# Performance work log

Measured on AMD Instinct MI355X. Metric: run time of the kernel, lower is better.

Reference implementation:

```python
import jax, jax.numpy as jnp
import numpy as np

NUM_HEADS = 16
HEAD_DIM = 64  # v_emb_out // num_heads


def setup_inputs() -> dict:
    key = jax.random.key(0)
    ks = jax.random.split(key, 12)
    B, QL, KL = 2, 2048, 2048
    D = 1024  # q_emb_in = k_emb_in = v_emb_in = v_emb_out
    s = 0.02
    return {
        "q": jax.random.normal(ks[0], (B, QL, D), jnp.float32),
        "k": jax.random.normal(ks[1], (B, KL, D), jnp.float32),
        "v": jax.random.normal(ks[2], (B, KL, D), jnp.float32),
        "mask": jnp.zeros((B, 1, 1, KL), jnp.int32),
        "Wq": jax.random.normal(ks[3], (D, D), jnp.float32) * s,
        "bq": jnp.zeros((D,), jnp.float32),
        "Wk": jax.random.normal(ks[4], (D, D), jnp.float32) * s,
        "bk": jnp.zeros((D,), jnp.float32),
        "Wv": jax.random.normal(ks[5], (D, D), jnp.float32) * s,
        "bv": jnp.zeros((D,), jnp.float32),
        "Wo": jax.random.normal(ks[6], (D, D), jnp.float32) * s,
        "bo": jnp.zeros((D,), jnp.float32),
    }


def _split_heads(x):
    # (B, S, D) -> (B, H, S, Hd)
    B, S, D = x.shape
    return x.reshape(B, S, NUM_HEADS, HEAD_DIM).transpose(0, 2, 1, 3)


def reference(q, k, v, mask, Wq, bq, Wk, bk, Wv, bv, Wo, bo):
    Q = _split_heads(q @ Wq.T + bq)
    K = _split_heads(k @ Wk.T + bk)
    V = _split_heads(v @ Wv.T + bv)
    scores = jnp.einsum("bhqd,bhkd->bhqk", Q, K) / jnp.sqrt(
        jnp.asarray(HEAD_DIM, Q.dtype)
    )
    scores = jnp.where(mask.astype(bool), jnp.asarray(-jnp.inf, scores.dtype), scores)
    attn = jax.nn.softmax(scores, axis=-1)
    out = jnp.einsum("bhqk,bhkd->bhqd", attn, V)  # (B,H,Q,Hd)
    B, H, QL, Hd = out.shape
    out = out.transpose(0, 2, 1, 3).reshape(B, QL, H * Hd)
    return out @ Wo.T + bo
```

## Files before the change

### kernel.cpp

```cpp
#include <hip/hip_runtime.h>
#include <hip/hip_bf16.h>
#include <math.h>
#include <stdint.h>


typedef __bf16 bf16x8 __attribute__((ext_vector_type(8)));
typedef float  f32x4  __attribute__((ext_vector_type(4)));
typedef float  f32x8  __attribute__((ext_vector_type(8)));
typedef float  f32x16 __attribute__((ext_vector_type(16)));
typedef unsigned int   u32x4 __attribute__((ext_vector_type(4)));
typedef unsigned short u16x8 __attribute__((ext_vector_type(8)));
typedef unsigned short u16x4 __attribute__((ext_vector_type(4)));
typedef u16x8 u16x8a __attribute__((may_alias));
typedef u16x4 u16x4a __attribute__((may_alias));
typedef f32x8 f32x8a __attribute__((may_alias));
typedef unsigned short u16a __attribute__((may_alias));
typedef float f32a __attribute__((may_alias));

#define BATCH 2
#define SQL   2048
#define DM    1024
#define NH    16
#define HD    64

__device__ __forceinline__ unsigned short f2bf(float f) {
    union { __hip_bfloat16 h; unsigned short u; } cv;
    cv.h = __float2bfloat16(f);
    return cv.u;
}
__device__ __forceinline__ float bf2f(unsigned short u) {
    union { unsigned int i; float f; } cv;
    cv.i = ((unsigned int)u) << 16;
    return cv.f;
}
__device__ __forceinline__ bf16x8 ldfrag(const unsigned short* p) {
    return __builtin_bit_cast(bf16x8, *(const u16x8a*)p);
}
__device__ __forceinline__ void stage8(const void* __restrict__ src, size_t off,
                                       int f32f, unsigned short* dst) {
    if (f32f) {
        f32x8 v = *(const f32x8a*)((const float*)src + off);
        u16x8 o;
#pragma unroll
        for (int i = 0; i < 8; i++) o[i] = f2bf(v[i]);
        *(u16x8a*)dst = o;
    } else {
        *(u16x8a*)dst = *(const u16x8a*)((const unsigned short*)src + off);
    }
}
__device__ __forceinline__ float rdel(const void* p, size_t i, int f) {
    return f ? ((const f32a*)p)[i] : bf2f(((const u16a*)p)[i]);
}
__device__ __forceinline__ void gload16(const void* g, void* l) {
    __builtin_amdgcn_global_load_lds(
        (const __attribute__((address_space(1))) unsigned int*)g,
        (__attribute__((address_space(3))) unsigned int*)l,
        16, 0, 0);
}
__device__ __forceinline__ unsigned int cvtpk(float lo, float hi) {
    unsigned int r;
    asm("v_cvt_pk_bf16_f32 %0, %1, %2" : "=v"(r) : "v"(lo), "v"(hi));
    return r;
}
__device__ __forceinline__ float fexp2(float x) {
#if __has_builtin(__builtin_amdgcn_exp2f)
    return __builtin_amdgcn_exp2f(x);
#else
    float r;
    asm("v_exp_f32 %0, %1" : "=v"(r) : "v"(x));
    return r;
#endif
}

__global__ void sniff(const void* __restrict__ q, int* __restrict__ flag) {
    __shared__ int cnt;
    if (threadIdx.x == 0) cnt = 0;
    __syncthreads();
    const u16a* p = (const u16a*)q;
    int c = 0;
#pragma unroll
    for (int i = 0; i < 8; i++) {
        unsigned short u = p[threadIdx.x * 8 + i];
        int e = (u >> 7) & 0xFF;
        if (e >= 96 && e <= 159) c++;
    }
    atomicAdd(&cnt, c);
    __syncthreads();
    if (threadIdx.x == 0) *flag = (cnt < 1741) ? 1 : 0;
}

__global__ __launch_bounds__(256)
void convert(const void* s0, const void* s1, const void* s2, const void* s3,
             const void* s4, const void* s5, const void* s6,
             unsigned short* d0, unsigned short* d1, unsigned short* d2,
             unsigned short* d3, unsigned short* d4, unsigned short* d5,
             unsigned short* d6, const int* __restrict__ flag)
{
    if (*flag == 0) return;
    const int z = blockIdx.z;
    const float* s; unsigned short* d; size_t n;
    switch (z) {
        case 0: s = (const float*)s0; d = d0; n = (size_t)BATCH * SQL * DM; break;
        case 1: s = (const float*)s1; d = d1; n = (size_t)BATCH * SQL * DM; break;
        case 2: s = (const float*)s2; d = d2; n = (size_t)BATCH * SQL * DM; break;
        case 3: s = (const float*)s3; d = d3; n = (size_t)DM * DM; break;
        case 4: s = (const float*)s4; d = d4; n = (size_t)DM * DM; break;
        case 5: s = (const float*)s5; d = d5; n = (size_t)DM * DM; break;
        default: s = (const float*)s6; d = d6; n = (size_t)DM * DM; break;
    }
    const size_t stride = (size_t)gridDim.x * blockDim.x * 8;
    for (size_t i = ((size_t)blockIdx.x * blockDim.x + threadIdx.x) * 8; i < n;
         i += stride) {
        f32x8 v = *(const f32x8a*)(s + i);
        u16x8 o;
#pragma unroll
        for (int j = 0; j < 8; j++) o[j] = f2bf(v[j]);
        *(u16x8a*)(d + i) = o;
    }
}

template<int BLDS, int BN>
__device__ __forceinline__ void gemm_core(
    const unsigned short* __restrict__ Abf,
    const unsigned short* __restrict__ Bbf,
    const void* __restrict__ Braw,
    const void* __restrict__ bias, void* __restrict__ Cv,
    float scale, int wF32, int oMode, int bF32)
{
    constexpr int K = 1024, N = 1024, BK = 32;
    constexpr int NJ = BN / 32;
    constexpr int CALLS = BN / 64;
    __shared__ unsigned short Alds[128 * BK];
    __shared__ unsigned short Blds[BN * BK];

    const int t = threadIdx.x;
    const int lane = t & 63, wave = t >> 6;
    const int quad = lane >> 4, r15 = lane & 15;
    const int wm = (wave >> 1) * 64, wn = (wave & 1) * (BN / 2);
    const int m0 = blockIdx.x * 128, n0 = blockIdx.y * BN;

    f32x4 acc[4][NJ];
#pragma unroll
    for (int i = 0; i < 4; i++)
#pragma unroll
        for (int j = 0; j < NJ; j++) acc[i][j] = (f32x4){0.f, 0.f, 0.f, 0.f};

    const int gr = lane >> 2, gc = lane & 3;
    const unsigned short* gA = Abf + (size_t)(m0 + wave * 32 + gr) * K + gc * 8;
    const unsigned short* gB = Bbf + (size_t)(n0 + wave * 16 * CALLS + gr) * K + gc * 8;
    unsigned short* lA = &Alds[wave * 1024];
    unsigned short* lB = &Blds[wave * 512 * CALLS];
    const int srow = t >> 2, sch = t & 3;
    const size_t offB0 = (size_t)(n0 + srow) * K + sch * 8;
    const size_t offB1 = (size_t)(n0 + 64 + srow) * K + sch * 8;

    for (int k0 = 0; k0 < K; k0 += BK) {
        gload16(gA + k0, lA);
        gload16(gA + k0 + 16 * K, lA + 512);
        if constexpr (BLDS) {
#pragma unroll
            for (int c = 0; c < CALLS; c++)
                gload16(gB + k0 + c * 16 * K, lB + c * 512);
        } else {
            stage8(Braw, offB0 + k0, wF32, &Blds[srow * BK + sch * 8]);
            if constexpr (BN == 128)
                stage8(Braw, offB1 + k0, wF32, &Blds[(64 + srow) * BK + sch * 8]);
        }
        __syncthreads();

        bf16x8 af[4], bfr[NJ];
#pragma unroll
        for (int i = 0; i < 4; i++)
            af[i] = ldfrag(&Alds[(wm + i * 16 + r15) * BK + quad * 8]);
#pragma unroll
        for (int j = 0; j < NJ; j++)
            bfr[j] = ldfrag(&Blds[(wn + j * 16 + r15) * BK + quad * 8]);
#pragma unroll
        for (int i = 0; i < 4; i++)
#pragma unroll
            for (int j = 0; j < NJ; j++)
                acc[i][j] = __builtin_amdgcn_mfma_f32_16x16x32_bf16(af[i], bfr[j], acc[i][j], 0, 0, 0);
        __syncthreads();
    }

    float bvv[NJ];
#pragma unroll
    for (int j = 0; j < NJ; j++)
        bvv[j] = rdel(bias, n0 + wn + j * 16 + r15, bF32);

    if (oMode == 2) {
#pragma unroll
        for (int i = 0; i < 4; i++)
#pragma unroll
            for (int j = 0; j < NJ; j++) {
                int rr = m0 + wm + i * 16 + quad * 4;
                int cc = n0 + wn + j * 16 + r15;
                int bb = rr >> 11, tok = rr & (SQL - 1);
                int hh = cc >> 6,  dd  = cc & (HD - 1);
                u16x4 pk;
#pragma unroll
                for (int r = 0; r < 4; r++) pk[r] = f2bf(acc[i][j][r] + bvv[j]);
                *(u16x4a*)&((u16a*)Cv)[((((size_t)bb * NH + hh) * HD + dd) << 11) + tok] = pk;
            }
    } else {
#pragma unroll
        for (int i = 0; i < 4; i++)
#pragma unroll
            for (int j = 0; j < NJ; j++)
#pragma unroll
                for (int r = 0; r < 4; r++) {
                    int rr = m0 + wm + i * 16 + quad * 4 + r;
                    int cc = n0 + wn + j * 16 + r15;
                    float vv = (acc[i][j][r] + bvv[j]) * scale;
                    if (oMode) ((f32a*)Cv)[(size_t)rr * N + cc] = vv;
                    else       ((u16a*)Cv)[(size_t)rr * N + cc] = f2bf(vv);
                }
    }
}

template<int BLDS>
__global__ __launch_bounds__(256)
void gemm_qkv_k(const void* __restrict__ xq, const void* __restrict__ xk,
                const void* __restrict__ xv,
                const unsigned short* __restrict__ qc,
                const unsigned short* __restrict__ kc,
                const unsigned short* __restrict__ vc,
                const void* __restrict__ Wq, const void* __restrict__ Wk,
                const void* __restrict__ Wv,
                const unsigned short* __restrict__ Wqc,
                const unsigned short* __restrict__ Wkc,
                const unsigned short* __restrict__ Wvc,
                const void* __restrict__ bq, const void* __restrict__ bk,
                const void* __restrict__ bv,
                unsigned short* __restrict__ Qp, unsigned short* __restrict__ Kp,
                unsigned short* __restrict__ Vp,
                float qscale, const int* __restrict__ flag)
{
    const int f = *flag;
    const int z = blockIdx.z;
    const void* xo = (z == 0) ? xq : (z == 1) ? xk : xv;
    const unsigned short* xc = (z == 0) ? qc : (z == 1) ? kc : vc;
    const unsigned short* A = f ? xc : (const unsigned short*)xo;
    const void* Wraw = (z == 0) ? Wq : (z == 1) ? Wk : Wv;
    const unsigned short* Wc = (z == 0) ? Wqc : (z == 1) ? Wkc : Wvc;
    const unsigned short* Bc = (BLDS && f) ? Wc : (const unsigned short*)Wraw;
    const void* bi = (z == 0) ? bq : (z == 1) ? bk : bv;
    unsigned short* C = (z == 0) ? Qp : (z == 1) ? Kp : Vp;
    gemm_core<BLDS, 128>(A, Bc, Wraw, bi, C, (z == 0) ? qscale : 1.0f, f,
                         (z == 2) ? 2 : 0, f);
}

template<int BLDS>
__global__ __launch_bounds__(256)
void gemm_o_k(const unsigned short* __restrict__ A, const void* __restrict__ Wo,
              const unsigned short* __restrict__ Woc, const void* __restrict__ bo,
              void* __restrict__ out, const int* __restrict__ flag)
{
    const int f = *flag;
    const unsigned short* Bc = (BLDS && f) ? Woc : (const unsigned short*)Wo;
    gemm_core<BLDS, 64>(A, Bc, Wo, bo, out, 1.0f, f, f, f);
}

__global__ __launch_bounds__(256)
void flash(const unsigned short* __restrict__ Qp,
           const unsigned short* __restrict__ Kp,
           const unsigned short* __restrict__ VT,
           const int* __restrict__ mask,
           unsigned short* __restrict__ AO)
{
    __shared__ unsigned short Klds[2][64 * 64];
    __shared__ unsigned short Vlds[2][64 * 64];

    const int t = threadIdx.x, wave = t >> 6, lane = t & 63;
    const int hi = lane >> 5, l31 = lane & 31;
    const int x7 = l31 & 7;
    const int lin = blockIdx.x + 16 * blockIdx.y;
    const int xcd = lin & 7, jj = lin >> 3;
    const int bh = xcd + 8 * (jj >> 4);
    const int qt = jj & 15;
    const int b = bh >> 4, h = bh & 15;
    const size_t base = (size_t)b * SQL * DM + (size_t)h * HD;

    const int srow8 = lane >> 3, sc8 = lane & 7;
    const unsigned short* gK[2];
    const unsigned short* gV[2];
    int ldof[2];
#pragma unroll
    for (int i = 0; i < 2; i++) {
        const int row = wave * 16 + i * 8 + srow8;
        const int slot = sc8 ^ (row & 7);
        gK[i] = Kp + base + (size_t)row * DM + slot * 8;
        gV[i] = VT + (((size_t)(b * NH + h) * HD + row) << 11) + slot * 8;
        ldof[i] = (wave * 16 + i * 8) * 64;
    }

    const int qrow = qt * 128 + wave * 32 + l31;
    bf16x8 qf[4];
#pragma unroll
    for (int c = 0; c < 4; c++)
        qf[c] = ldfrag(&Qp[base + (size_t)qrow * DM + c * 16 + hi * 8]);

    f32x16 o0 = {}, o1 = {};
    float l_acc = 0.f;

#pragma unroll
    for (int i = 0; i < 2; i++) {
        gload16(gK[i], &Klds[0][ldof[i]]);
        gload16(gV[i], &Vlds[0][ldof[i]]);
    }
    __syncthreads();

    constexpr int NT = SQL / 64;
    for (int it = 0; it < NT; ++it) {
        const int bs = it & 1;
        const int n0 = it * 64;

        const int mk = mask[b * SQL + n0 + lane];

        if (it + 1 < NT) {
#pragma unroll
            for (int i = 0; i < 2; i++) {
                gload16(gK[i] + (size_t)(n0 + 64) * DM, &Klds[bs ^ 1][ldof[i]]);
                gload16(gV[i] + (n0 + 64),              &Vlds[bs ^ 1][ldof[i]]);
            }
        }

        f32x16 s0 = {}, s1 = {};
#pragma unroll
        for (int c = 0; c < 4; c++) {
            const int sl = (((c * 2 + hi) ^ x7) << 3);
            bf16x8 kf0 = ldfrag(&Klds[bs][l31 * 64 + sl]);
            bf16x8 kf1 = ldfrag(&Klds[bs][(32 + l31) * 64 + sl]);
            s0 = __builtin_amdgcn_mfma_f32_32x32x16_bf16(kf0, qf[c], s0, 0, 0, 0);
            s1 = __builtin_amdgcn_mfma_f32_32x32x16_bf16(kf1, qf[c], s1, 0, 0, 0);
        }

        const unsigned long long bal = __ballot(mk != 0);

#pragma unroll
        for (int r = 0; r < 16; r++) {
            s0[r] = fexp2(s0[r]);
            s1[r] = fexp2(s1[r]);
        }
        if (__builtin_expect(bal != 0ull, 0)) {
            const unsigned int m0 = ((unsigned int)bal) >> (4 * hi);
            const unsigned int m1 = ((unsigned int)(bal >> 32)) >> (4 * hi);
#pragma unroll
            for (int r = 0; r < 16; r++) {
                const int bp = ((r >> 2) << 3) + (r & 3);
                if ((m0 >> bp) & 1) s0[r] = 0.f;
                if ((m1 >> bp) & 1) s1[r] = 0.f;
            }
        }
#pragma unroll
        for (int r = 0; r < 16; r++) l_acc += s0[r] + s1[r];

#pragma unroll
        for (int c = 0; c < 4; c++) {
            const int qb = 2 * (c & 1);
            unsigned int x0, x1, y0, y1;
            if (c < 2) {
                x0 = cvtpk(s0[4 * qb + 0], s0[4 * qb + 1]);
                x1 = cvtpk(s0[4 * qb + 2], s0[4 * qb + 3]);
                y0 = cvtpk(s0[4 * qb + 4], s0[4 * qb + 5]);
                y1 = cvtpk(s0[4 * qb + 6], s0[4 * qb + 7]);
            } else {
                x0 = cvtpk(s1[4 * qb + 0], s1[4 * qb + 1]);
                x1 = cvtpk(s1[4 * qb + 2], s1[4 * qb + 3]);
                y0 = cvtpk(s1[4 * qb + 4], s1[4 * qb + 5]);
                y1 = cvtpk(s1[4 * qb + 6], s1[4 * qb + 7]);
            }
            asm volatile("v_permlane32_swap_b32 %0, %1" : "+v"(x0), "+v"(y0));
            asm volatile("v_permlane32_swap_b32 %0, %1" : "+v"(x1), "+v"(y1));
            u32x4 w = {x0, x1, y0, y1};
            bf16x8 pa = __builtin_bit_cast(bf16x8, w);

            const int sl = (((c * 2 + hi) ^ x7) << 3);
            bf16x8 v0 = ldfrag(&Vlds[bs][l31 * 64 + sl]);
            bf16x8 v1 = ldfrag(&Vlds[bs][(32 + l31) * 64 + sl]);
            o0 = __builtin_amdgcn_mfma_f32_32x32x16_bf16(pa, v0, o0, 0, 0, 0);
            o1 = __builtin_amdgcn_mfma_f32_32x32x16_bf16(pa, v1, o1, 0, 0, 0);
        }
        __syncthreads();
    }

    const float l_tot = l_acc + __shfl_xor(l_acc, 32, 64);
    const float linv = (l_tot > 0.f) ? 1.0f / l_tot : 0.f;

#pragma unroll
    for (int r = 0; r < 16; r++) {
        const int ql = (r & 3) + ((r >> 2) << 3) + 4 * hi;
        const float ls = __shfl(linv, ql, 64);
        const int row = qt * 128 + wave * 32 + ql;
        AO[base + (size_t)row * DM + l31]      = f2bf(o0[r] * ls);
        AO[base + (size_t)row * DM + 32 + l31] = f2bf(o1[r] * ls);
    }
}

extern "C" void kernel_launch(void* const* d_in, const int* in_sizes, int n_in,
                              void* d_out, int out_size, void* d_ws, size_t ws_size,
                              hipStream_t stream)
{
    (void)in_sizes; (void)n_in; (void)out_size;

    const void* q    = d_in[0];
    const void* k    = d_in[1];
    const void* v    = d_in[2];
    const int*  mask = (const int*)d_in[3];
    const void* Wq   = d_in[4];
    const void* bq   = d_in[5];
    const void* Wk   = d_in[6];
    const void* bk   = d_in[7];
    const void* Wv   = d_in[8];
    const void* bv   = d_in[9];
    const void* Wo   = d_in[10];
    const void* bo   = d_in[11];

    const size_t ACT = (size_t)BATCH * SQL * DM;
    const size_t WE  = (size_t)DM * DM;
    int* flag = (int*)d_ws;
    unsigned short* Qp = (unsigned short*)((char*)d_ws + 512);
    unsigned short* Kp = Qp + ACT;
    unsigned short* Vp = Kp + ACT;
    unsigned short* AO = Vp + ACT;

    const size_t needFull = 512 + (4 * ACT + 3 * ACT + 4 * WE) * 2;
    const size_t needMid  = 512 + (4 * ACT + 4 * WE) * 2;
    const int tier = (ws_size >= needFull) ? 2 : (ws_size >= needMid) ? 1 : 0;

    unsigned short* qc;
    unsigned short* kc;
    unsigned short* vc;
    unsigned short* Wqc = AO + ACT;
    unsigned short* Wkc = Wqc + WE;
    unsigned short* Wvc = Wkc + WE;
    unsigned short* Woc = Wvc + WE;
    if (tier == 2) {
        qc = Woc + WE;
        kc = qc + ACT;
        vc = kc + ACT;
    } else {
        qc = AO;
        kc = (unsigned short*)d_out;
        vc = kc + ACT;
    }

    const float QSCALE = 0.125f * 1.44269504088896340736f;

    sniff<<<1, 256, 0, stream>>>(q, flag);
    if (tier >= 1) {
        convert<<<dim3(256, 1, 7), 256, 0, stream>>>(
            q, k, v, Wq, Wk, Wv, Wo, qc, kc, vc, Wqc, Wkc, Wvc, Woc, flag);
        gemm_qkv_k<1><<<dim3(32, 8, 3), 256, 0, stream>>>(
            q, k, v, qc, kc, vc, Wq, Wk, Wv, Wqc, Wkc, Wvc,
            bq, bk, bv, Qp, Kp, Vp, QSCALE, flag);
    } else {
        convert<<<dim3(256, 1, 3), 256, 0, stream>>>(
            q, k, v, nullptr, nullptr, nullptr, nullptr,
            qc, kc, vc, nullptr, nullptr, nullptr, nullptr, flag);
        gemm_qkv_k<0><<<dim3(32, 8, 3), 256, 0, stream>>>(
            q, k, v, qc, kc, vc, Wq, Wk, Wv, nullptr, nullptr, nullptr,
            bq, bk, bv, Qp, Kp, Vp, QSCALE, flag);
    }
    flash<<<dim3(SQL / 128, BATCH * NH), 256, 0, stream>>>(Qp, Kp, Vp, mask, AO);
    if (tier >= 1)
        gemm_o_k<1><<<dim3(32, 16), 256, 0, stream>>>(AO, Wo, Woc, bo, d_out, flag);
    else
        gemm_o_k<0><<<dim3(32, 16), 256, 0, stream>>>(AO, Wo, nullptr, bo, d_out, flag);
}
```

Measured before the change: 234.7 us.

## Triple-buffer K/V tiles and software-pipeline QK^T ahead of softmax-PV in flash

Replaces the double-buffered flash loop with a three-stage ring of K/V LDS buffers and a software pipeline that computes the next tile's QK^T MFMAs before doing softmax and PV for the current tile. This overlaps exp/convert work with matrix ops and gives loads more time to land. It also changes the LDS XOR swizzle to mix in row>>3, which is meant to cut bank conflicts on fragment reads. In exchange it uses more LDS and registers for the second score accumulator pair, which may lower occupancy.

```diff
diff --git a/kernel.cpp b/kernel.cpp
--- a/kernel.cpp
+++ b/kernel.cpp
@@ -268,12 +268,13 @@
            const int* __restrict__ mask,
            unsigned short* __restrict__ AO)
 {
-    __shared__ unsigned short Klds[2][64 * 64];
-    __shared__ unsigned short Vlds[2][64 * 64];
+    __shared__ unsigned short Klds[3][64 * 64];
+    __shared__ unsigned short Vlds[3][64 * 64];
 
     const int t = threadIdx.x, wave = t >> 6, lane = t & 63;
     const int hi = lane >> 5, l31 = lane & 31;
-    const int x7 = l31 & 7;
+    const int kq0 = (l31 ^ (l31 >> 3)) & 7;
+    const int kq1 = kq0 ^ 4;
     const int lin = blockIdx.x + 16 * blockIdx.y;
     const int xcd = lin & 7, jj = lin >> 3;
     const int bh = xcd + 8 * (jj >> 4);
@@ -288,7 +289,7 @@
 #pragma unroll
     for (int i = 0; i < 2; i++) {
         const int row = wave * 16 + i * 8 + srow8;
-        const int slot = sc8 ^ (row & 7);
+        const int slot = sc8 ^ ((row ^ (row >> 3)) & 7);
         gK[i] = Kp + base + (size_t)row * DM + slot * 8;
         gV[i] = VT + (((size_t)(b * NH + h) * HD + row) << 11) + slot * 8;
         ldof[i] = (wave * 16 + i * 8) * 64;
@@ -303,44 +304,28 @@
     f32x16 o0 = {}, o1 = {};
     float l_acc = 0.f;
 
-#pragma unroll
-    for (int i = 0; i < 2; i++) {
-        gload16(gK[i], &Klds[0][ldof[i]]);
-        gload16(gV[i], &Vlds[0][ldof[i]]);
-    }
-    __syncthreads();
-
-    constexpr int NT = SQL / 64;
-    for (int it = 0; it < NT; ++it) {
-        const int bs = it & 1;
-        const int n0 = it * 64;
-
-        const int mk = mask[b * SQL + n0 + lane];
-
-        if (it + 1 < NT) {
-#pragma unroll
-            for (int i = 0; i < 2; i++) {
-                gload16(gK[i] + (size_t)(n0 + 64) * DM, &Klds[bs ^ 1][ldof[i]]);
-                gload16(gV[i] + (n0 + 64),              &Vlds[bs ^ 1][ldof[i]]);
-            }
-        }
-
-        f32x16 s0 = {}, s1 = {};
+    auto STAGE = [&](int tile, int bi) {
+#pragma unroll
+        for (int i = 0; i < 2; i++) {
+            gload16(gK[i] + (size_t)tile * 64 * DM, &Klds[bi][ldof[i]]);
+            gload16(gV[i] + tile * 64,              &Vlds[bi][ldof[i]]);
+        }
+    };
+    auto QKT = [&](int bi, f32x16& S0, f32x16& S1) {
 #pragma unroll
         for (int c = 0; c < 4; c++) {
-            const int sl = (((c * 2 + hi) ^ x7) << 3);
-            bf16x8 kf0 = ldfrag(&Klds[bs][l31 * 64 + sl]);
-            bf16x8 kf1 = ldfrag(&Klds[bs][(32 + l31) * 64 + sl]);
-            s0 = __builtin_amdgcn_mfma_f32_32x32x16_bf16(kf0, qf[c], s0, 0, 0, 0);
-            s1 = __builtin_amdgcn_mfma_f32_32x32x16_bf16(kf1, qf[c], s1, 0, 0, 0);
-        }
-
-        const unsigned long long bal = __ballot(mk != 0);
-
+            const int ch = c * 2 + hi;
+            bf16x8 kf0 = ldfrag(&Klds[bi][l31 * 64 + ((ch ^ kq0) << 3)]);
+            bf16x8 kf1 = ldfrag(&Klds[bi][(32 + l31) * 64 + ((ch ^ kq1) << 3)]);
+            S0 = __builtin_amdgcn_mfma_f32_32x32x16_bf16(kf0, qf[c], S0, 0, 0, 0);
+            S1 = __builtin_amdgcn_mfma_f32_32x32x16_bf16(kf1, qf[c], S1, 0, 0, 0);
+        }
+    };
+    auto SMPV = [&](f32x16& S0, f32x16& S1, int bi, unsigned long long bal) {
 #pragma unroll
         for (int r = 0; r < 16; r++) {
-            s0[r] = fexp2(s0[r]);
-            s1[r] = fexp2(s1[r]);
+            S0[r] = fexp2(S0[r]);
+            S1[r] = fexp2(S1[r]);
         }
         if (__builtin_expect(bal != 0ull, 0)) {
             const unsigned int m0 = ((unsigned int)bal) >> (4 * hi);
@@ -348,40 +333,69 @@
 #pragma unroll
             for (int r = 0; r < 16; r++) {
                 const int bp = ((r >> 2) << 3) + (r & 3);
-                if ((m0 >> bp) & 1) s0[r] = 0.f;
-                if ((m1 >> bp) & 1) s1[r] = 0.f;
+                if ((m0 >> bp) & 1) S0[r] = 0.f;
+                if ((m1 >> bp) & 1) S1[r] = 0.f;
             }
         }
 #pragma unroll
-        for (int r = 0; r < 16; r++) l_acc += s0[r] + s1[r];
-
+        for (int r = 0; r < 16; r++) l_acc += S0[r] + S1[r];
 #pragma unroll
         for (int c = 0; c < 4; c++) {
             const int qb = 2 * (c & 1);
             unsigned int x0, x1, y0, y1;
             if (c < 2) {
-                x0 = cvtpk(s0[4 * qb + 0], s0[4 * qb + 1]);
-                x1 = cvtpk(s0[4 * qb + 2], s0[4 * qb + 3]);
-                y0 = cvtpk(s0[4 * qb + 4], s0[4 * qb + 5]);
-                y1 = cvtpk(s0[4 * qb + 6], s0[4 * qb + 7]);
+                x0 = cvtpk(S0[4 * qb + 0], S0[4 * qb + 1]);
+                x1 = cvtpk(S0[4 * qb + 2], S0[4 * qb + 3]);
+                y0 = cvtpk(S0[4 * qb + 4], S0[4 * qb + 5]);
+                y1 = cvtpk(S0[4 * qb + 6], S0[4 * qb + 7]);
             } else {
-                x0 = cvtpk(s1[4 * qb + 0], s1[4 * qb + 1]);
-                x1 = cvtpk(s1[4 * qb + 2], s1[4 * qb + 3]);
-                y0 = cvtpk(s1[4 * qb + 4], s1[4 * qb + 5]);
-                y1 = cvtpk(s1[4 * qb + 6], s1[4 * qb + 7]);
+                x0 = cvtpk(S1[4 * qb + 0], S1[4 * qb + 1]);
+                x1 = cvtpk(S1[4 * qb + 2], S1[4 * qb + 3]);
+                y0 = cvtpk(S1[4 * qb + 4], S1[4 * qb + 5]);
+                y1 = cvtpk(S1[4 * qb + 6], S1[4 * qb + 7]);
             }
             asm volatile("v_permlane32_swap_b32 %0, %1" : "+v"(x0), "+v"(y0));
             asm volatile("v_permlane32_swap_b32 %0, %1" : "+v"(x1), "+v"(y1));
             u32x4 w = {x0, x1, y0, y1};
             bf16x8 pa = __builtin_bit_cast(bf16x8, w);
 
-            const int sl = (((c * 2 + hi) ^ x7) << 3);
-            bf16x8 v0 = ldfrag(&Vlds[bs][l31 * 64 + sl]);
-            bf16x8 v1 = ldfrag(&Vlds[bs][(32 + l31) * 64 + sl]);
+            const int ch = c * 2 + hi;
+            bf16x8 v0 = ldfrag(&Vlds[bi][l31 * 64 + ((ch ^ kq0) << 3)]);
+            bf16x8 v1 = ldfrag(&Vlds[bi][(32 + l31) * 64 + ((ch ^ kq1) << 3)]);
             o0 = __builtin_amdgcn_mfma_f32_32x32x16_bf16(pa, v0, o0, 0, 0, 0);
             o1 = __builtin_amdgcn_mfma_f32_32x32x16_bf16(pa, v1, o1, 0, 0, 0);
         }
+    };
+
+    constexpr int NT = SQL / 64;
+    STAGE(0, 0);
+    __syncthreads();
+    STAGE(1, 1);
+    int mkC = mask[b * SQL + lane];
+    f32x16 sA0 = {}, sA1 = {}, sB0 = {}, sB1 = {};
+    QKT(0, sA0, sA1);
+
+    for (int tt = 0; tt < NT; tt += 2) {
         __syncthreads();
+        if (tt + 2 < NT) STAGE(tt + 2, (tt + 2) % 3);
+        int mkN = (tt + 1 < NT) ? mask[b * SQL + (tt + 1) * 64 + lane] : 0;
+        if (tt + 1 < NT) {
+            sB0 = 0.f; sB1 = 0.f;
+            QKT((tt + 1) % 3, sB0, sB1);
+        }
+        unsigned long long bal = __ballot(mkC != 0);
+        SMPV(sA0, sA1, tt % 3, bal);
+        mkC = mkN;
+        __syncthreads();
+        if (tt + 3 < NT) STAGE(tt + 3, (tt + 3) % 3);
+        mkN = (tt + 2 < NT) ? mask[b * SQL + (tt + 2) * 64 + lane] : 0;
+        if (tt + 2 < NT) {
+            sA0 = 0.f; sA1 = 0.f;
+            QKT((tt + 2) % 3, sA0, sA1);
+        }
+        bal = __ballot(mkC != 0);
+        SMPV(sB0, sB1, (tt + 1) % 3, bal);
+        mkC = mkN;
     }
 
     const float l_tot = l_acc + __shfl_xor(l_acc, 32, 64);
```

Result: faster. 226.3 us (-3.6%).
